# Optimization experiments

Measured on AMD Instinct MI355X. Metric: run time of the kernel, lower is better.

Reference implementation:

```python
import jax, jax.numpy as jnp
import numpy as np


def setup_inputs() -> dict:
    key = jax.random.key(0)
    k1, k2, k3, k4 = jax.random.split(key, 4)
    B, C, H, Wd = 32, 512, 32, 32
    sparse_dim, dict_size, feature_dim = 1024, 1024, 512
    x = jax.random.normal(k1, (B, C, H, Wd), dtype=jnp.float32)
    dictionary = jax.random.normal(k2, (dict_size, feature_dim), dtype=jnp.float32)
    # scale W, S like the LISTA init (|| . || ~ O(1)) so iterates stay bounded
    W = jax.random.normal(k3, (sparse_dim, feature_dim), dtype=jnp.float32) * 0.02
    S = jax.random.normal(k4, (sparse_dim, sparse_dim), dtype=jnp.float32) * 0.02
    thresh = jnp.float32(0.1)
    return {"x": x, "dictionary": dictionary, "W": W, "S": S, "thresh": thresh, "num_steps": 5}


def _soft_threshold(z, thresh):
    return jnp.sign(z) * jnp.maximum(jnp.abs(z) - thresh, 0.0)


def reference(x, dictionary, W, S, thresh, num_steps):
    B, C, H, Wd = x.shape
    sparse_dim = S.shape[0]
    # [B,C,H,W] -> [B*H*W, C]
    x_flat = jnp.transpose(x, (0, 2, 3, 1)).reshape(-1, C)
    dict_norm = dictionary / jnp.linalg.norm(dictionary, axis=1, keepdims=True)
    # W @ x^T is loop-invariant; compute once. [K, N]
    Wx = W @ x_flat.T
    z = jnp.zeros((sparse_dim, x_flat.shape[0]), dtype=x.dtype)
    for _ in range(num_steps):
        z = z + Wx
        z = z - S @ z
        z = _soft_threshold(z, thresh)
    # [K,N] -> [B,K,H,W]
    z = jnp.transpose(z.T.reshape(B, H, Wd, sparse_dim), (0, 3, 1, 2))
    return (z, dict_norm)
```

## Files before the change

### kernel.cpp

```cpp
#include <hip/hip_runtime.h>
#include <hip/hip_bf16.h>

typedef __bf16 bf16_t;
typedef __bf16 bf16x4 __attribute__((ext_vector_type(4)));
typedef __bf16 bf16x8 __attribute__((ext_vector_type(8)));
typedef float f32x4 __attribute__((ext_vector_type(4)));

#define GLOAD_LDS16(g, l)                                                      \
  __builtin_amdgcn_global_load_lds(                                            \
      (const __attribute__((address_space(1))) void*)(g),                      \
      (__attribute__((address_space(3))) void*)(l), 16, 0, 0)

#define MFMA(a, b, c) __builtin_amdgcn_mfma_f32_16x16x32_bf16((a), (b), (c), 0, 0, 0)

__global__ __launch_bounds__(512, 2) void gemm_kernel(
    const bf16_t* __restrict__ A, const bf16_t* __restrict__ Bt,
    int Kd, int mode,
    const bf16_t* __restrict__ WxIn, bf16_t* __restrict__ UnextOrWx,
    float* __restrict__ Out, const float* __restrict__ thresh_p)
{
  __shared__ __align__(16) char smem[147456];
  bf16_t* lds = (bf16_t*)smem;

  const int tid = threadIdx.x;
  const int wid = tid >> 6, lane = tid & 63;
  const int wr = wid >> 1, wc = wid & 1;
  const int lr = lane & 15, kg = lane >> 4;

  const int per = gridDim.x >> 3;
  const int logical = (blockIdx.x & 7) * per + (blockIdx.x >> 3);
  const int tileN = (logical & 7) << 7;
  const int tileM = (logical >> 3) << 8;
  const int NT = Kd >> 6;

  size_t offA[4]; int dstA[4];
  #pragma unroll
  for (int j = 0; j < 4; ++j) {
    const int f = j * 512 + tid;
    const int row = f >> 3, u = f & 7;
    const int ug = u ^ (row & 7);
    offA[j] = (size_t)(tileM + row) * Kd + ug * 8;
    dstA[j] = f * 8;
  }
  size_t offB[2]; int dstB[2];
  #pragma unroll
  for (int j = 0; j < 2; ++j) {
    const int f = j * 512 + tid;
    const int col = f >> 3, u = f & 7;
    const int ug = u ^ (col & 7);
    offB[j] = (size_t)(tileN + col) * Kd + ug * 8;
    dstB[j] = 16384 + f * 8;
  }

  auto readA = [&](int mi, int ks, int bs) -> bf16x8 {
    const int R = wr * 64 + mi * 16 + lr;
    const int ul = (ks * 4 + kg) ^ (R & 7);
    return *(const bf16x8*)(lds + bs + R * 64 + ul * 8);
  };
  auto readB = [&](int ni, int ks, int bs) -> bf16x8 {
    const int C = wc * 64 + ni * 16 + lr;
    const int ul = (ks * 4 + kg) ^ (C & 7);
    return *(const bf16x8*)(lds + bs + 16384 + C * 64 + ul * 8);
  };

  f32x4 acc[4][4] = {};
  bf16x8 a0[4], b0[4], a1[4], b1[4];

  #pragma unroll
  for (int j = 0; j < 4; ++j) GLOAD_LDS16(A + offA[j], lds + dstA[j]);
  #pragma unroll
  for (int j = 0; j < 2; ++j) GLOAD_LDS16(Bt + offB[j], lds + dstB[j]);
  if (NT > 1) {
    #pragma unroll
    for (int j = 0; j < 4; ++j) GLOAD_LDS16(A + offA[j] + 64, lds + 24576 + dstA[j]);
    #pragma unroll
    for (int j = 0; j < 2; ++j) GLOAD_LDS16(Bt + offB[j] + 64, lds + 24576 + dstB[j]);
  }
  asm volatile("s_waitcnt vmcnt(6)" ::: "memory");
  __syncthreads();

  int buf = 0, sb3 = 2;
  for (int t = 0; t < NT; ++t) {
    const int bs = buf * 24576;
    const int sbs = sb3 * 24576;
    const int ts = (t + 2 < NT) ? t + 2 : t + 2 - NT;
    const size_t ko = (size_t)ts << 6;

    GLOAD_LDS16(A + offA[0] + ko, lds + sbs + dstA[0]);
    GLOAD_LDS16(A + offA[1] + ko, lds + sbs + dstA[1]);
    GLOAD_LDS16(A + offA[2] + ko, lds + sbs + dstA[2]);
    GLOAD_LDS16(A + offA[3] + ko, lds + sbs + dstA[3]);
    GLOAD_LDS16(Bt + offB[0] + ko, lds + sbs + dstB[0]);
    GLOAD_LDS16(Bt + offB[1] + ko, lds + sbs + dstB[1]);

    #pragma unroll
    for (int mi = 0; mi < 4; ++mi) a0[mi] = readA(mi, 0, bs);
    #pragma unroll
    for (int ni = 0; ni < 4; ++ni) b0[ni] = readB(ni, 0, bs);
    #pragma unroll
    for (int mi = 0; mi < 4; ++mi) a1[mi] = readA(mi, 1, bs);
    #pragma unroll
    for (int ni = 0; ni < 4; ++ni) b1[ni] = readB(ni, 1, bs);

    #pragma unroll
    for (int mi = 0; mi < 4; ++mi)
      #pragma unroll
      for (int ni = 0; ni < 4; ++ni)
        acc[mi][ni] = MFMA(a0[mi], b0[ni], acc[mi][ni]);
    #pragma unroll
    for (int mi = 0; mi < 4; ++mi)
      #pragma unroll
      for (int ni = 0; ni < 4; ++ni)
        acc[mi][ni] = MFMA(a1[mi], b1[ni], acc[mi][ni]);

    asm volatile("s_waitcnt vmcnt(6)" ::: "memory");
    __syncthreads();

    buf = (buf == 2) ? 0 : buf + 1;
    sb3 = (sb3 == 2) ? 0 : sb3 + 1;
  }

  const float th = *thresh_p;

  if (mode <= 1) {
    asm volatile("s_waitcnt vmcnt(0)" ::: "memory");
    __syncthreads();
    float* Tl = (float*)smem;
    #pragma unroll
    for (int c = 0; c < 8; ++c) {
      if (c) __syncthreads();
      if (wr == (c >> 1)) {
        #pragma unroll
        for (int mj = 0; mj < 2; ++mj) {
          const int mi = (c & 1) * 2 + mj;
          const int rl = mj * 16 + kg * 4;
          #pragma unroll
          for (int ni = 0; ni < 4; ++ni) {
            const int cl = wc * 64 + ni * 16 + lr;
            #pragma unroll
            for (int r = 0; r < 4; ++r)
              Tl[(rl + r) * 132 + cl] = acc[mi][ni][r];
          }
        }
      }
      __syncthreads();
      #pragma unroll
      for (int j = 0; j < 2; ++j) {
        const int f  = j * 512 + tid;
        const int rl = f >> 5;
        const int c4 = (f & 31) * 4;
        const f32x4 v = *(const f32x4*)&Tl[rl * 132 + c4];
        const int grow = tileM + c * 32 + rl;
        const size_t gidx = (size_t)grow * 1024 + tileN + c4;
        bf16x4 ov;
        if (mode == 1) {
          const bf16x4 wx = *(const bf16x4*)&WxIn[gidx];
          #pragma unroll
          for (int e = 0; e < 4; ++e) {
            const float a  = fabsf(v[e]) - th;
            const float zn = (a > 0.f) ? copysignf(a, v[e]) : 0.f;
            ov[e] = (bf16_t)(zn + (float)wx[e]);
          }
        } else {
          #pragma unroll
          for (int e = 0; e < 4; ++e) ov[e] = (bf16_t)v[e];
        }
        *(bf16x4*)&UnextOrWx[gidx] = ov;
      }
    }
  } else {
    #pragma unroll
    for (int mi = 0; mi < 4; ++mi)
      #pragma unroll
      for (int ni = 0; ni < 4; ++ni)
        #pragma unroll
        for (int r = 0; r < 4; ++r) {
          const float v = acc[mi][ni][r];
          const float a = fabsf(v) - th;
          acc[mi][ni][r] = (a > 0.f) ? copysignf(a, v) : 0.f;
        }
    asm volatile("s_waitcnt vmcnt(0)" ::: "memory");
    __syncthreads();
    float* T = (float*)smem;
    const int    bb    = tileM >> 10;
    const size_t obase = (size_t)bb * 1048576 + (size_t)(tileM & 1023);
    #pragma unroll
    for (int ch = 0; ch < 4; ++ch) {
      if (ch) __syncthreads();
      if (wc == (ch >> 1)) {
        #pragma unroll
        for (int nj = 0; nj < 2; ++nj) {
          const int ni = (ch & 1) * 2 + nj;
          const int cp = nj * 16 + lr;
          #pragma unroll
          for (int mi = 0; mi < 4; ++mi)
            #pragma unroll
            for (int r = 0; r < 4; ++r)
              T[cp * 260 + wr * 64 + mi * 16 + kg * 4 + r] = acc[mi][ni][r];
        }
      }
      __syncthreads();
      #pragma unroll
      for (int j = 0; j < 4; ++j) {
        const int f  = j * 512 + tid;
        const int cp = f >> 6;
        const int p4 = (f & 63) * 4;
        const f32x4 v = *(const f32x4*)&T[cp * 260 + p4];
        *(f32x4*)&Out[obase + (size_t)(tileN + ch * 32 + cp) * 1024 + p4] = v;
      }
    }
  }
}

__global__ void cast_f32_bf16_kernel(const float* __restrict__ src,
                                     bf16_t* __restrict__ dst, int n) {
  int i = blockIdx.x * blockDim.x + threadIdx.x;
  if (i < n) dst[i] = (bf16_t)src[i];
}

__global__ void make_T_kernel(const float* __restrict__ S,
                              bf16_t* __restrict__ T) {
  const int idx = blockIdx.x * blockDim.x + threadIdx.x;
  const int i = idx >> 10, j = idx & 1023;
  T[idx] = (bf16_t)(((i == j) ? 1.0f : 0.0f) - S[idx]);
}

__global__ void transpose_cast_x_kernel(const float* __restrict__ x,
                                        bf16_t* __restrict__ xt) {
  __shared__ float t[32][33];
  const int b  = blockIdx.z;
  const int p0 = blockIdx.x * 32;
  const int c0 = blockIdx.y * 32;
  const int tx = threadIdx.x, ty = threadIdx.y;
  #pragma unroll
  for (int i = 0; i < 32; i += 8)
    t[ty + i][tx] = x[((size_t)b * 512 + c0 + ty + i) * 1024 + p0 + tx];
  __syncthreads();
  #pragma unroll
  for (int i = 0; i < 32; i += 8)
    xt[((size_t)b * 1024 + p0 + ty + i) * 512 + c0 + tx] = (bf16_t)t[tx][ty + i];
}

__global__ void dict_norm_kernel(const float* __restrict__ dict,
                                 float* __restrict__ out) {
  const int row = blockIdx.x;
  const int tid = threadIdx.x;
  const float* r = dict + (size_t)row * 512;
  float s = 0.f;
  for (int i = tid; i < 512; i += 256) { float v = r[i]; s += v * v; }
  #pragma unroll
  for (int off = 32; off > 0; off >>= 1) s += __shfl_down(s, off);
  __shared__ float ps[4];
  if ((tid & 63) == 0) ps[tid >> 6] = s;
  __syncthreads();
  const float inv = 1.0f / sqrtf(ps[0] + ps[1] + ps[2] + ps[3]);
  for (int i = tid; i < 512; i += 256) out[(size_t)row * 512 + i] = r[i] * inv;
}

extern "C" void kernel_launch(void* const* d_in, const int* in_sizes, int n_in,
                              void* d_out, int out_size, void* d_ws, size_t ws_size,
                              hipStream_t stream) {
  const float* x      = (const float*)d_in[0];
  const float* dict   = (const float*)d_in[1];
  const float* W      = (const float*)d_in[2];
  const float* S      = (const float*)d_in[3];
  const float* thresh = (const float*)d_in[4];

  float* out = (float*)d_out;

  char* ws = (char*)d_ws;
  bf16_t* uA   = (bf16_t*)ws;
  bf16_t* uB   = (bf16_t*)(ws + 67108864);
  bf16_t* WxBf = (bf16_t*)(ws + 134217728);
  bf16_t* xt   = (bf16_t*)(ws + 201326592);
  bf16_t* Wbf  = (bf16_t*)(ws + 234881024);
  bf16_t* Tbf  = (bf16_t*)(ws + 235929600);

  float* dnorm = out + 33554432;

  cast_f32_bf16_kernel<<<dim3(2048), dim3(256), 0, stream>>>(W, Wbf, 524288);
  make_T_kernel<<<dim3(2048), dim3(512), 0, stream>>>(S, Tbf);
  transpose_cast_x_kernel<<<dim3(32, 16, 32), dim3(32, 8), 0, stream>>>(x, xt);
  dict_norm_kernel<<<dim3(1024), dim3(256), 0, stream>>>(dict, dnorm);

  gemm_kernel<<<dim3(1024), dim3(512), 0, stream>>>(
      xt, Wbf, 512, 0, nullptr, WxBf, nullptr, thresh);

  bf16_t* uc = WxBf; bf16_t* un = uA;
  for (int s = 0; s < 4; ++s) {
    gemm_kernel<<<dim3(1024), dim3(512), 0, stream>>>(
        uc, Tbf, 1024, 1, WxBf, un, nullptr, thresh);
    uc = un;
    un = (uc == uA) ? uB : uA;
  }
  gemm_kernel<<<dim3(1024), dim3(512), 0, stream>>>(
      uc, Tbf, 1024, 2, nullptr, nullptr, out, thresh);
}
```

Before: 558.0 us.

## Precompute (I-S)·W to shrink the first LISTA iteration GEMM to K=512

New measurement: 542.1 us. 1.03x faster.

```diff
diff --git a/kernel.cpp b/kernel.cpp
--- a/kernel.cpp
+++ b/kernel.cpp
@@ -15,7 +15,7 @@
 
 __global__ __launch_bounds__(512, 2) void gemm_kernel(
     const bf16_t* __restrict__ A, const bf16_t* __restrict__ Bt,
-    int Kd, int mode,
+    int Kd, int Nc, int mode,
     const bf16_t* __restrict__ WxIn, bf16_t* __restrict__ UnextOrWx,
     float* __restrict__ Out, const float* __restrict__ thresh_p)
 {
@@ -29,8 +29,9 @@
 
   const int per = gridDim.x >> 3;
   const int logical = (blockIdx.x & 7) * per + (blockIdx.x >> 3);
-  const int tileN = (logical & 7) << 7;
-  const int tileM = (logical >> 3) << 8;
+  const int ntn = Nc >> 7;
+  const int tileN = (logical % ntn) << 7;
+  const int tileM = (logical / ntn) << 8;
   const int NT = Kd >> 6;
 
   size_t offA[4]; int dstA[4];
@@ -77,7 +78,7 @@
     for (int j = 0; j < 2; ++j) GLOAD_LDS16(Bt + offB[j] + 64, lds + 24576 + dstB[j]);
   }
   asm volatile("s_waitcnt vmcnt(6)" ::: "memory");
-  __syncthreads();
+  __builtin_amdgcn_s_barrier();
 
   int buf = 0, sb3 = 2;
   for (int t = 0; t < NT; ++t) {
@@ -114,7 +115,7 @@
         acc[mi][ni] = MFMA(a1[mi], b1[ni], acc[mi][ni]);
 
     asm volatile("s_waitcnt vmcnt(6)" ::: "memory");
-    __syncthreads();
+    __builtin_amdgcn_s_barrier();
 
     buf = (buf == 2) ? 0 : buf + 1;
     sb3 = (sb3 == 2) ? 0 : sb3 + 1;
@@ -151,7 +152,7 @@
         const int c4 = (f & 31) * 4;
         const f32x4 v = *(const f32x4*)&Tl[rl * 132 + c4];
         const int grow = tileM + c * 32 + rl;
-        const size_t gidx = (size_t)grow * 1024 + tileN + c4;
+        const size_t gidx = (size_t)grow * Nc + tileN + c4;
         bf16x4 ov;
         if (mode == 1) {
           const bf16x4 wx = *(const bf16x4*)&WxIn[gidx];
@@ -181,7 +182,7 @@
         }
     asm volatile("s_waitcnt vmcnt(0)" ::: "memory");
     __syncthreads();
-    float* T = (float*)smem;
+    float* Tl = (float*)smem;
     const int    bb    = tileM >> 10;
     const size_t obase = (size_t)bb * 1048576 + (size_t)(tileM & 1023);
     #pragma unroll
@@ -196,7 +197,7 @@
           for (int mi = 0; mi < 4; ++mi)
             #pragma unroll
             for (int r = 0; r < 4; ++r)
-              T[cp * 260 + wr * 64 + mi * 16 + kg * 4 + r] = acc[mi][ni][r];
+              Tl[cp * 260 + wr * 64 + mi * 16 + kg * 4 + r] = acc[mi][ni][r];
         }
       }
       __syncthreads();
@@ -205,24 +206,21 @@
         const int f  = j * 512 + tid;
         const int cp = f >> 6;
         const int p4 = (f & 63) * 4;
-        const f32x4 v = *(const f32x4*)&T[cp * 260 + p4];
+        const f32x4 v = *(const f32x4*)&Tl[cp * 260 + p4];
         *(f32x4*)&Out[obase + (size_t)(tileN + ch * 32 + cp) * 1024 + p4] = v;
       }
     }
   }
 }
 
-__global__ void cast_f32_bf16_kernel(const float* __restrict__ src,
-                                     bf16_t* __restrict__ dst, int n) {
-  int i = blockIdx.x * blockDim.x + threadIdx.x;
-  if (i < n) dst[i] = (bf16_t)src[i];
-}
-
-__global__ void make_T_kernel(const float* __restrict__ S,
-                              bf16_t* __restrict__ T) {
+__global__ void make_T_castW_kernel(const float* __restrict__ S,
+                                    bf16_t* __restrict__ T,
+                                    const float* __restrict__ W,
+                                    bf16_t* __restrict__ Wb) {
   const int idx = blockIdx.x * blockDim.x + threadIdx.x;
   const int i = idx >> 10, j = idx & 1023;
   T[idx] = (bf16_t)(((i == j) ? 1.0f : 0.0f) - S[idx]);
+  if (idx < 524288) Wb[idx] = (bf16_t)W[idx];
 }
 
 __global__ void transpose_cast_x_kernel(const float* __restrict__ x,
@@ -239,6 +237,21 @@
   #pragma unroll
   for (int i = 0; i < 32; i += 8)
     xt[((size_t)b * 1024 + p0 + ty + i) * 512 + c0 + tx] = (bf16_t)t[tx][ty + i];
+}
+
+__global__ void transpose_cast_w_kernel(const float* __restrict__ W,
+                                        bf16_t* __restrict__ Wt) {
+  __shared__ float t[32][33];
+  const int j0 = blockIdx.x * 32;
+  const int c0 = blockIdx.y * 32;
+  const int tx = threadIdx.x, ty = threadIdx.y;
+  #pragma unroll
+  for (int i = 0; i < 32; i += 8)
+    t[ty + i][tx] = W[(size_t)(j0 + ty + i) * 512 + c0 + tx];
+  __syncthreads();
+  #pragma unroll
+  for (int i = 0; i < 32; i += 8)
+    Wt[(size_t)(c0 + ty + i) * 1024 + j0 + tx] = (bf16_t)t[tx][ty + i];
 }
 
 __global__ void dict_norm_kernel(const float* __restrict__ dict,
@@ -276,23 +289,30 @@
   bf16_t* Wbf  = (bf16_t*)(ws + 234881024);
   bf16_t* Tbf  = (bf16_t*)(ws + 235929600);
 
+  bf16_t* WtBf = (bf16_t*)out;
+  bf16_t* TWbf = WtBf + 524288;
   float* dnorm = out + 33554432;
 
-  cast_f32_bf16_kernel<<<dim3(2048), dim3(256), 0, stream>>>(W, Wbf, 524288);
-  make_T_kernel<<<dim3(2048), dim3(512), 0, stream>>>(S, Tbf);
+  make_T_castW_kernel<<<dim3(2048), dim3(512), 0, stream>>>(S, Tbf, W, Wbf);
   transpose_cast_x_kernel<<<dim3(32, 16, 32), dim3(32, 8), 0, stream>>>(x, xt);
+  transpose_cast_w_kernel<<<dim3(32, 16), dim3(32, 8), 0, stream>>>(W, WtBf);
   dict_norm_kernel<<<dim3(1024), dim3(256), 0, stream>>>(dict, dnorm);
 
+  gemm_kernel<<<dim3(16), dim3(512), 0, stream>>>(
+      Tbf, WtBf, 1024, 512, 0, nullptr, TWbf, nullptr, thresh);
+
   gemm_kernel<<<dim3(1024), dim3(512), 0, stream>>>(
-      xt, Wbf, 512, 0, nullptr, WxBf, nullptr, thresh);
-
-  bf16_t* uc = WxBf; bf16_t* un = uA;
-  for (int s = 0; s < 4; ++s) {
+      xt, Wbf, 512, 1024, 0, nullptr, WxBf, nullptr, thresh);
+
+  gemm_kernel<<<dim3(1024), dim3(512), 0, stream>>>(
+      xt, TWbf, 512, 1024, 1, WxBf, uA, nullptr, thresh);
+
+  bf16_t* uc = uA; bf16_t* un = uB;
+  for (int s = 0; s < 3; ++s) {
     gemm_kernel<<<dim3(1024), dim3(512), 0, stream>>>(
-        uc, Tbf, 1024, 1, WxBf, un, nullptr, thresh);
-    uc = un;
-    un = (uc == uA) ? uB : uA;
+        uc, Tbf, 1024, 1024, 1, WxBf, un, nullptr, thresh);
+    bf16_t* tmp = uc; uc = un; un = tmp;
   }
   gemm_kernel<<<dim3(1024), dim3(512), 0, stream>>>(
-      uc, Tbf, 1024, 2, nullptr, nullptr, out, thresh);
-}
+      uc, Tbf, 1024, 1024, 2, nullptr, nullptr, out, thresh);
+}
```
